# Optimization experiments

Hardware: AMD Instinct MI355X
Metric: run time of the kernel (lower is better)

## Reference

```python
import jax, jax.numpy as jnp
import numpy as np

B, N = 256, 512
DIM_GRAPH = 256
DIM_DESC = 256
RANK = 64


def setup_inputs() -> dict:
    key = jax.random.key(0)
    ks = jax.random.split(key, 6)
    tokns_k = jax.random.normal(ks[0], (B, DIM_DESC), dtype=jnp.float32)
    H_pad = jax.random.normal(ks[1], (B, N, DIM_GRAPH), dtype=jnp.float32)
    mask = jax.random.randint(ks[2], (B, N), 0, 2).astype(bool)
    mask = mask.at[:, 0].set(True)  # ensure at least one valid node per graph
    # Linear weights, torch convention: y = x @ W.T
    Wq = jax.random.normal(ks[3], (RANK, DIM_DESC), dtype=jnp.float32) / np.sqrt(DIM_DESC)
    Wk = jax.random.normal(ks[4], (RANK, DIM_GRAPH), dtype=jnp.float32) / np.sqrt(DIM_GRAPH)
    Wv = jax.random.normal(ks[5], (DIM_DESC, DIM_GRAPH), dtype=jnp.float32) / np.sqrt(DIM_GRAPH)
    log_scale = jnp.zeros((1,), dtype=jnp.float32)
    return {"tokns_k": tokns_k, "H_pad": H_pad, "mask": mask,
            "Wq": Wq, "Wk": Wk, "Wv": Wv, "log_scale": log_scale}


def reference(tokns_k, H_pad, mask, Wq, Wk, Wv, log_scale):
    q = tokns_k @ Wq.T                                  # [B, r]
    k = jnp.einsum('bnd,rd->bnr', H_pad, Wk)            # [B, N, r]
    scale = jnp.maximum(jnp.exp(log_scale), 0.1)        # clamp(min=0.1)
    scores = jnp.einsum('br,bnr->bn', q, k) / scale     # [B, N]
    neg_inf = jnp.float32(-jnp.inf)
    scores = jnp.where(mask, scores, neg_inf)
    alpha = jax.nn.softmax(scores, axis=-1)             # [B, N]
    v = jnp.einsum('bnd,ed->bne', H_pad, Wv)            # [B, N, dim_desc]
    ctx_k = jnp.einsum('bn,bne->be', alpha, v)          # [B, dim_desc]
    return (alpha, ctx_k)
```

## Files before the change

### kernel.cpp

```cpp
#include <hip/hip_runtime.h>

constexpr int Bc = 256;
constexpr int Nc = 512;
constexpr int Dc = 256;
constexpr int Rc = 64;
constexpr int NT = 1024;
constexpr int NW = NT / 64;
constexpr int ROWS_PER_WAVE = Nc / NW;
constexpr int STEPS = ROWS_PER_WAVE / 4;
constexpr int NPART = NW * 4;

__global__ __launch_bounds__(NT) void fba_kernel(
    const float* __restrict__ tokns_k,
    const float* __restrict__ H_pad,
    const int*   __restrict__ mask,
    const float* __restrict__ Wq,
    const float* __restrict__ Wk,
    const float* __restrict__ Wv,
    const float* __restrict__ log_scale,
    float*       __restrict__ out)
{
    const int b    = blockIdx.x;
    const int t    = threadIdx.x;
    const int wave = t >> 6;
    const int lane = t & 63;
    const int g    = lane >> 4;
    const int l16  = lane & 15;

    __shared__ __align__(16) float q_s[Rc];
    __shared__ __align__(16) float p_s[Dc];
    __shared__ __align__(16) float scores_s[Nc];
    __shared__ float l_s[NPART];
    __shared__ __align__(16) float hm[NPART][Dc];
    __shared__ __align__(16) float tmp4[4][Dc];
    __shared__ __align__(16) float hbar[Dc];
    __shared__ int   mask_s[Nc];

    const float inv_scale = 1.0f / fmaxf(__expf(log_scale[0]), 0.1f);

    {
        const int r = wave * 4 + g;
        float acc = 0.0f;
        #pragma unroll
        for (int j = 0; j < 4; ++j) {
            const float4 tk = *(const float4*)(tokns_k + b * Dc + l16 * 4 + j * 64);
            const float4 wq = *(const float4*)(Wq + r * Dc + l16 * 4 + j * 64);
            acc += tk.x * wq.x + tk.y * wq.y + tk.z * wq.z + tk.w * wq.w;
        }
        #pragma unroll
        for (int off = 1; off < 16; off <<= 1) acc += __shfl_xor(acc, off);
        if (l16 == 0) q_s[r] = acc;
    }
    if (t < Nc) mask_s[t] = mask[b * Nc + t];
    __syncthreads();

    {
        const int d = t & 255, quarter = t >> 8;
        float acc = 0.0f;
        #pragma unroll
        for (int i = 0; i < 16; ++i) {
            const int r = quarter * 16 + i;
            acc += q_s[r] * Wk[r * Dc + d];
        }
        tmp4[quarter][d] = acc;
    }
    __syncthreads();
    if (t < Dc) p_s[t] = (tmp4[0][t] + tmp4[1][t]) + (tmp4[2][t] + tmp4[3][t]);
    __syncthreads();

    float4 p4[4];
    #pragma unroll
    for (int j = 0; j < 4; ++j) p4[j] = *(const float4*)(p_s + l16 * 4 + j * 64);

    const float* __restrict__ Hb = H_pad + (size_t)b * Nc * Dc;
    float  l_acc = 0.0f;
    float4 h4[4];
    #pragma unroll
    for (int j = 0; j < 4; ++j) h4[j] = make_float4(0.f, 0.f, 0.f, 0.f);

    #pragma unroll
    for (int step = 0; step < STEPS; ++step) {
        const int n = wave * ROWS_PER_WAVE + step * 4 + g;
        const float* __restrict__ row = Hb + n * Dc + l16 * 4;
        float4 x[4];
        #pragma unroll
        for (int j = 0; j < 4; ++j) x[j] = *(const float4*)(row + j * 64);

        float s0 = x[0].x * p4[0].x + x[0].y * p4[0].y + x[0].z * p4[0].z + x[0].w * p4[0].w;
        float s1 = x[1].x * p4[1].x + x[1].y * p4[1].y + x[1].z * p4[1].z + x[1].w * p4[1].w;
        float s2 = x[2].x * p4[2].x + x[2].y * p4[2].y + x[2].z * p4[2].z + x[2].w * p4[2].w;
        float s3 = x[3].x * p4[3].x + x[3].y * p4[3].y + x[3].z * p4[3].z + x[3].w * p4[3].w;
        float s = (s0 + s1) + (s2 + s3);
        #pragma unroll
        for (int off = 1; off < 16; off <<= 1) s += __shfl_xor(s, off);
        s *= inv_scale;
        if (mask_s[n] == 0) s = -1e30f;
        if (l16 == 0) scores_s[n] = s;

        const float pn = __expf(s);
        l_acc += pn;
        #pragma unroll
        for (int j = 0; j < 4; ++j) {
            h4[j].x = fmaf(pn, x[j].x, h4[j].x);
            h4[j].y = fmaf(pn, x[j].y, h4[j].y);
            h4[j].z = fmaf(pn, x[j].z, h4[j].z);
            h4[j].w = fmaf(pn, x[j].w, h4[j].w);
        }
    }

    const int pw = wave * 4 + g;
    #pragma unroll
    for (int j = 0; j < 4; ++j) *(float4*)(&hm[pw][l16 * 4 + j * 64]) = h4[j];
    if (l16 == 0) l_s[pw] = l_acc;
    __syncthreads();

    float L = 0.0f;
    #pragma unroll
    for (int p = 0; p < NPART; ++p) L += l_s[p];
    const float invL = 1.0f / L;

    {
        const int col = t & 255, quarter = t >> 8;
        float acc = 0.0f;
        #pragma unroll
        for (int i = 0; i < 16; ++i) acc += hm[quarter * 16 + i][col];
        tmp4[quarter][col] = acc;
    }
    if (t < Nc) out[b * Nc + t] = __expf(scores_s[t]) * invL;
    __syncthreads();
    if (t < Dc) hbar[t] = ((tmp4[0][t] + tmp4[1][t]) + (tmp4[2][t] + tmp4[3][t])) * invL;
    __syncthreads();

    float4 hb4[4];
    #pragma unroll
    for (int j = 0; j < 4; ++j) hb4[j] = *(const float4*)(hbar + l16 * 4 + j * 64);
    float* __restrict__ ctx_out = out + Bc * Nc + b * Dc;
    #pragma unroll
    for (int step = 0; step < 4; ++step) {
        const int e = wave * 16 + step * 4 + g;
        float acc = 0.0f;
        #pragma unroll
        for (int j = 0; j < 4; ++j) {
            const float4 wv = *(const float4*)(Wv + e * Dc + l16 * 4 + j * 64);
            acc += wv.x * hb4[j].x + wv.y * hb4[j].y + wv.z * hb4[j].z + wv.w * hb4[j].w;
        }
        #pragma unroll
        for (int off = 1; off < 16; off <<= 1) acc += __shfl_xor(acc, off);
        if (l16 == 0) ctx_out[e] = acc;
    }
}

extern "C" void kernel_launch(void* const* d_in, const int* in_sizes, int n_in,
                              void* d_out, int out_size, void* d_ws, size_t ws_size,
                              hipStream_t stream) {
    const float* tokns_k   = (const float*)d_in[0];
    const float* H_pad     = (const float*)d_in[1];
    const int*   mask      = (const int*)d_in[2];
    const float* Wq        = (const float*)d_in[3];
    const float* Wk        = (const float*)d_in[4];
    const float* Wv        = (const float*)d_in[5];
    const float* log_scale = (const float*)d_in[6];
    float* out = (float*)d_out;

    fba_kernel<<<Bc, NT, 0, stream>>>(tokns_k, H_pad, mask, Wq, Wk, Wv, log_scale, out);
}
```

Baseline: 224.0 us.

## Split attention over N into three kernels with workspace merge

```diff
diff --git a/kernel.cpp b/kernel.cpp
--- a/kernel.cpp
+++ b/kernel.cpp
@@ -4,42 +4,27 @@
 constexpr int Nc = 512;
 constexpr int Dc = 256;
 constexpr int Rc = 64;
-constexpr int NT = 1024;
-constexpr int NW = NT / 64;
-constexpr int ROWS_PER_WAVE = Nc / NW;
-constexpr int STEPS = ROWS_PER_WAVE / 4;
-constexpr int NPART = NW * 4;
-
-__global__ __launch_bounds__(NT) void fba_kernel(
-    const float* __restrict__ tokns_k,
-    const float* __restrict__ H_pad,
-    const int*   __restrict__ mask,
-    const float* __restrict__ Wq,
-    const float* __restrict__ Wk,
-    const float* __restrict__ Wv,
-    const float* __restrict__ log_scale,
-    float*       __restrict__ out)
-{
-    const int b    = blockIdx.x;
-    const int t    = threadIdx.x;
-    const int wave = t >> 6;
-    const int lane = t & 63;
-    const int g    = lane >> 4;
-    const int l16  = lane & 15;
-
-    __shared__ __align__(16) float q_s[Rc];
-    __shared__ __align__(16) float p_s[Dc];
-    __shared__ __align__(16) float scores_s[Nc];
-    __shared__ float l_s[NPART];
-    __shared__ __align__(16) float hm[NPART][Dc];
-    __shared__ __align__(16) float tmp4[4][Dc];
-    __shared__ __align__(16) float hbar[Dc];
-    __shared__ int   mask_s[Nc];
-
-    const float inv_scale = 1.0f / fmaxf(__expf(log_scale[0]), 0.1f);
-
-    {
-        const int r = wave * 4 + g;
+constexpr int SPLIT = 8;
+constexpr int ROWS = Nc / SPLIT;
+
+constexpr size_t WS_P = 0;
+constexpr size_t WS_L = WS_P + (size_t)Bc * Dc;
+constexpr size_t WS_H = WS_L + (size_t)Bc * SPLIT;
+constexpr size_t WS_FLOATS = WS_H + (size_t)Bc * SPLIT * Dc;
+
+__global__ __launch_bounds__(256) void k0_precompute_p(
+    const float* __restrict__ tokns_k, const float* __restrict__ Wq,
+    const float* __restrict__ Wk, float* __restrict__ ws)
+{
+    const int b = blockIdx.x;
+    const int t = threadIdx.x;
+    const int wave = t >> 6, lane = t & 63, g = lane >> 4, l16 = lane & 15;
+
+    __shared__ float q_s[Rc];
+
+    #pragma unroll
+    for (int step = 0; step < 4; ++step) {
+        const int r = wave * 16 + step * 4 + g;
         float acc = 0.0f;
         #pragma unroll
         for (int j = 0; j < 4; ++j) {
@@ -51,37 +36,50 @@
         for (int off = 1; off < 16; off <<= 1) acc += __shfl_xor(acc, off);
         if (l16 == 0) q_s[r] = acc;
     }
-    if (t < Nc) mask_s[t] = mask[b * Nc + t];
-    __syncthreads();
-
-    {
-        const int d = t & 255, quarter = t >> 8;
-        float acc = 0.0f;
-        #pragma unroll
-        for (int i = 0; i < 16; ++i) {
-            const int r = quarter * 16 + i;
-            acc += q_s[r] * Wk[r * Dc + d];
-        }
-        tmp4[quarter][d] = acc;
-    }
-    __syncthreads();
-    if (t < Dc) p_s[t] = (tmp4[0][t] + tmp4[1][t]) + (tmp4[2][t] + tmp4[3][t]);
-    __syncthreads();
-
+    __syncthreads();
+
+    float acc = 0.0f;
+    #pragma unroll 8
+    for (int r = 0; r < Rc; ++r) acc += q_s[r] * Wk[r * Dc + t];
+    ws[WS_P + (size_t)b * Dc + t] = acc;
+}
+
+__global__ __launch_bounds__(256) void k1_stream(
+    const float* __restrict__ H_pad, const int* __restrict__ mask,
+    const float* __restrict__ log_scale, float* __restrict__ ws,
+    float* __restrict__ out)
+{
+    const int s = blockIdx.x;
+    const int b = blockIdx.y;
+    const int t = threadIdx.x;
+    const int wave = t >> 6, lane = t & 63, g = lane >> 4, l16 = lane & 15;
+    const int n0 = s * ROWS;
+
+    __shared__ __align__(16) float hm[16][Dc];
+    __shared__ float l_s[16];
+    __shared__ float scores_s[ROWS];
+    __shared__ int   mask_s[ROWS];
+
+    if (t < ROWS) mask_s[t] = mask[b * Nc + n0 + t];
+
+    const float inv_scale = 1.0f / fmaxf(__expf(log_scale[0]), 0.1f);
+
+    const float* __restrict__ pb = ws + WS_P + (size_t)b * Dc;
     float4 p4[4];
     #pragma unroll
-    for (int j = 0; j < 4; ++j) p4[j] = *(const float4*)(p_s + l16 * 4 + j * 64);
-
-    const float* __restrict__ Hb = H_pad + (size_t)b * Nc * Dc;
+    for (int j = 0; j < 4; ++j) p4[j] = *(const float4*)(pb + l16 * 4 + j * 64);
+    __syncthreads();
+
+    const float* __restrict__ Hb = H_pad + ((size_t)b * Nc + n0) * Dc;
     float  l_acc = 0.0f;
     float4 h4[4];
     #pragma unroll
     for (int j = 0; j < 4; ++j) h4[j] = make_float4(0.f, 0.f, 0.f, 0.f);
 
     #pragma unroll
-    for (int step = 0; step < STEPS; ++step) {
-        const int n = wave * ROWS_PER_WAVE + step * 4 + g;
-        const float* __restrict__ row = Hb + n * Dc + l16 * 4;
+    for (int step = 0; step < 4; ++step) {
+        const int nr = step * 16 + wave * 4 + g;
+        const float* __restrict__ row = Hb + nr * Dc + l16 * 4;
         float4 x[4];
         #pragma unroll
         for (int j = 0; j < 4; ++j) x[j] = *(const float4*)(row + j * 64);
@@ -90,14 +88,14 @@
         float s1 = x[1].x * p4[1].x + x[1].y * p4[1].y + x[1].z * p4[1].z + x[1].w * p4[1].w;
         float s2 = x[2].x * p4[2].x + x[2].y * p4[2].y + x[2].z * p4[2].z + x[2].w * p4[2].w;
         float s3 = x[3].x * p4[3].x + x[3].y * p4[3].y + x[3].z * p4[3].z + x[3].w * p4[3].w;
-        float s = (s0 + s1) + (s2 + s3);
-        #pragma unroll
-        for (int off = 1; off < 16; off <<= 1) s += __shfl_xor(s, off);
-        s *= inv_scale;
-        if (mask_s[n] == 0) s = -1e30f;
-        if (l16 == 0) scores_s[n] = s;
-
-        const float pn = __expf(s);
+        float sc = (s0 + s1) + (s2 + s3);
+        #pragma unroll
+        for (int off = 1; off < 16; off <<= 1) sc += __shfl_xor(sc, off);
+        sc *= inv_scale;
+        if (mask_s[nr] == 0) sc = -1e30f;
+        if (l16 == 0) scores_s[nr] = sc;
+
+        const float pn = __expf(sc);
         l_acc += pn;
         #pragma unroll
         for (int j = 0; j < 4; ++j) {
@@ -108,36 +106,59 @@
         }
     }
 
-    const int pw = wave * 4 + g;
-    #pragma unroll
-    for (int j = 0; j < 4; ++j) *(float4*)(&hm[pw][l16 * 4 + j * 64]) = h4[j];
-    if (l16 == 0) l_s[pw] = l_acc;
-    __syncthreads();
+    const int team = wave * 4 + g;
+    #pragma unroll
+    for (int j = 0; j < 4; ++j) *(float4*)(&hm[team][l16 * 4 + j * 64]) = h4[j];
+    if (l16 == 0) l_s[team] = l_acc;
+    __syncthreads();
+
+    if (t < ROWS) out[b * Nc + n0 + t] = scores_s[t];
+    float hsum = 0.0f;
+    #pragma unroll
+    for (int p = 0; p < 16; ++p) hsum += hm[p][t];
+    ws[WS_H + ((size_t)b * SPLIT + s) * Dc + t] = hsum;
+    if (t == 0) {
+        float L = 0.0f;
+        #pragma unroll
+        for (int p = 0; p < 16; ++p) L += l_s[p];
+        ws[WS_L + (size_t)b * SPLIT + s] = L;
+    }
+}
+
+__global__ __launch_bounds__(256) void k2_merge(
+    const float* __restrict__ Wv, const float* __restrict__ ws,
+    float* __restrict__ out)
+{
+    const int b = blockIdx.x;
+    const int t = threadIdx.x;
+    const int wave = t >> 6, lane = t & 63, g = lane >> 4, l16 = lane & 15;
+
+    __shared__ __align__(16) float hbar[Dc];
 
     float L = 0.0f;
     #pragma unroll
-    for (int p = 0; p < NPART; ++p) L += l_s[p];
+    for (int s = 0; s < SPLIT; ++s) L += ws[WS_L + (size_t)b * SPLIT + s];
     const float invL = 1.0f / L;
 
-    {
-        const int col = t & 255, quarter = t >> 8;
-        float acc = 0.0f;
-        #pragma unroll
-        for (int i = 0; i < 16; ++i) acc += hm[quarter * 16 + i][col];
-        tmp4[quarter][col] = acc;
-    }
-    if (t < Nc) out[b * Nc + t] = __expf(scores_s[t]) * invL;
-    __syncthreads();
-    if (t < Dc) hbar[t] = ((tmp4[0][t] + tmp4[1][t]) + (tmp4[2][t] + tmp4[3][t])) * invL;
+    float hacc = 0.0f;
+    #pragma unroll
+    for (int s = 0; s < SPLIT; ++s) hacc += ws[WS_H + ((size_t)b * SPLIT + s) * Dc + t];
+    hbar[t] = hacc * invL;
+
+    #pragma unroll
+    for (int i = 0; i < Nc / 256; ++i) {
+        const int idx = b * Nc + i * 256 + t;
+        out[idx] = __expf(out[idx]) * invL;
+    }
     __syncthreads();
 
     float4 hb4[4];
     #pragma unroll
     for (int j = 0; j < 4; ++j) hb4[j] = *(const float4*)(hbar + l16 * 4 + j * 64);
-    float* __restrict__ ctx_out = out + Bc * Nc + b * Dc;
-    #pragma unroll
-    for (int step = 0; step < 4; ++step) {
-        const int e = wave * 16 + step * 4 + g;
+    float* __restrict__ ctx_out = out + (size_t)Bc * Nc + b * Dc;
+    #pragma unroll
+    for (int step = 0; step < 16; ++step) {
+        const int e = step * 16 + wave * 4 + g;
         float acc = 0.0f;
         #pragma unroll
         for (int j = 0; j < 4; ++j) {
@@ -147,6 +168,103 @@
         #pragma unroll
         for (int off = 1; off < 16; off <<= 1) acc += __shfl_xor(acc, off);
         if (l16 == 0) ctx_out[e] = acc;
+    }
+}
+
+constexpr int FNT = 512;
+constexpr int FNW = FNT / 64;
+constexpr int FNPW = Nc / FNW;
+
+__global__ __launch_bounds__(FNT) void fba_fallback(
+    const float* __restrict__ tokns_k, const float* __restrict__ H_pad,
+    const int* __restrict__ mask, const float* __restrict__ Wq,
+    const float* __restrict__ Wk, const float* __restrict__ Wv,
+    const float* __restrict__ log_scale, float* __restrict__ out)
+{
+    const int b = blockIdx.x, t = threadIdx.x;
+    const int wave = t >> 6, lane = t & 63;
+
+    __shared__ __align__(16) float q_s[Rc];
+    __shared__ __align__(16) float p_s[Dc];
+    __shared__ __align__(16) float scores_s[Nc];
+    __shared__ __align__(16) float hmerge[FNW][Dc];
+    __shared__ float l_s[FNW];
+    __shared__ __align__(16) float hbar[Dc];
+    __shared__ int mask_s[Nc];
+
+    const float inv_scale = 1.0f / fmaxf(__expf(log_scale[0]), 0.1f);
+
+    const float4 tok4 = *(const float4*)(tokns_k + b * Dc + lane * 4);
+    #pragma unroll
+    for (int i = 0; i < Rc / FNW; ++i) {
+        const int r = wave * (Rc / FNW) + i;
+        const float4 w4 = *(const float4*)(Wq + r * Dc + lane * 4);
+        float s = w4.x * tok4.x + w4.y * tok4.y + w4.z * tok4.z + w4.w * tok4.w;
+        #pragma unroll
+        for (int off = 32; off >= 1; off >>= 1) s += __shfl_xor(s, off);
+        if (lane == 0) q_s[r] = s;
+    }
+    mask_s[t] = mask[b * Nc + t];
+    mask_s[t + FNT] = mask[b * Nc + t + FNT];
+    __syncthreads();
+
+    if (t < Dc) {
+        float acc = 0.0f;
+        #pragma unroll 8
+        for (int r = 0; r < Rc; ++r) acc += q_s[r] * Wk[r * Dc + t];
+        p_s[t] = acc;
+    }
+    __syncthreads();
+
+    const float4 p4 = *(const float4*)(p_s + lane * 4);
+    const float* Hb = H_pad + (size_t)b * Nc * Dc;
+    float l_acc = 0.0f;
+    float4 h4 = make_float4(0.f, 0.f, 0.f, 0.f);
+
+    for (int i = 0; i < FNPW; ++i) {
+        const int n = wave * FNPW + i;
+        const float4 x4 = *(const float4*)(Hb + n * Dc + lane * 4);
+        float s = x4.x * p4.x + x4.y * p4.y + x4.z * p4.z + x4.w * p4.w;
+        #pragma unroll
+        for (int off = 32; off >= 1; off >>= 1) s += __shfl_xor(s, off);
+        s *= inv_scale;
+        if (mask_s[n] == 0) s = -1e30f;
+        if (lane == 0) scores_s[n] = s;
+        const float pn = __expf(s);
+        l_acc += pn;
+        h4.x = fmaf(pn, x4.x, h4.x); h4.y = fmaf(pn, x4.y, h4.y);
+        h4.z = fmaf(pn, x4.z, h4.z); h4.w = fmaf(pn, x4.w, h4.w);
+    }
+
+    if (lane == 0) l_s[wave] = l_acc;
+    *(float4*)(&hmerge[wave][lane * 4]) = h4;
+    __syncthreads();
+
+    float L = 0.0f;
+    #pragma unroll
+    for (int w = 0; w < FNW; ++w) L += l_s[w];
+    const float invL = 1.0f / L;
+
+    if (t < Dc) {
+        float acc = 0.0f;
+        #pragma unroll
+        for (int w = 0; w < FNW; ++w) acc += hmerge[w][t];
+        hbar[t] = acc * invL;
+    }
+    out[b * Nc + t] = __expf(scores_s[t]) * invL;
+    out[b * Nc + t + FNT] = __expf(scores_s[t + FNT]) * invL;
+    __syncthreads();
+
+    const float4 hb4 = *(const float4*)(hbar + lane * 4);
+    float* ctx_out = out + (size_t)Bc * Nc + b * Dc;
+    #pragma unroll
+    for (int i = 0; i < Dc / FNW; ++i) {
+        const int e = wave * (Dc / FNW) + i;
+        const float4 w4 = *(const float4*)(Wv + e * Dc + lane * 4);
+        float s = w4.x * hb4.x + w4.y * hb4.y + w4.z * hb4.z + w4.w * hb4.w;
+        #pragma unroll
+        for (int off = 32; off >= 1; off >>= 1) s += __shfl_xor(s, off);
+        if (lane == 0) ctx_out[e] = s;
     }
 }
 
@@ -162,5 +280,14 @@
     const float* log_scale = (const float*)d_in[6];
     float* out = (float*)d_out;
 
-    fba_kernel<<<Bc, NT, 0, stream>>>(tokns_k, H_pad, mask, Wq, Wk, Wv, log_scale, out);
-}
+    if (ws_size >= WS_FLOATS * sizeof(float)) {
+        float* ws = (float*)d_ws;
+        k0_precompute_p<<<Bc, 256, 0, stream>>>(tokns_k, Wq, Wk, ws);
+        dim3 grid1(SPLIT, Bc);
+        k1_stream<<<grid1, 256, 0, stream>>>(H_pad, mask, log_scale, ws, out);
+        k2_merge<<<Bc, 256, 0, stream>>>(Wv, ws, out);
+    } else {
+        fba_fallback<<<Bc, FNT, 0, stream>>>(tokns_k, H_pad, mask, Wq, Wk, Wv,
+                                             log_scale, out);
+    }
+}
```

Measured after the change: 223.3 us. Within noise of the previous version (-0.3%).
